# Performance work log

Hardware: AMD Instinct MI355X
Metric: run time of the kernel (lower is better)

The kernel has to match this reference:

```python
import jax, jax.numpy as jnp
import numpy as np

NUM_EXPERTS = 8
TOP_K = 2
HIDDEN = 2048
INTER = 2048
SWIGLU_LIMIT = 7.0
BATCH, SEQ = 4, 2048


def setup_inputs() -> dict:
    key = jax.random.key(0)
    k0, k1, k2, k3, k4 = jax.random.split(key, 5)
    x = jax.random.normal(k0, (BATCH, SEQ, HIDDEN), jnp.float32)
    Wr = jax.random.normal(k1, (HIDDEN, NUM_EXPERTS), jnp.float32) * 0.02
    Wg = jax.random.normal(k2, (NUM_EXPERTS, HIDDEN, INTER), jnp.float32) * 0.02
    Wu = jax.random.normal(k3, (NUM_EXPERTS, HIDDEN, INTER), jnp.float32) * 0.02
    Wd = jax.random.normal(k4, (NUM_EXPERTS, INTER, HIDDEN), jnp.float32) * 0.02
    return {"hidden_states": x, "Wr": Wr, "Wg": Wg, "Wu": Wu, "Wd": Wd}


def reference(hidden_states, Wr, Wg, Wu, Wd):
    # Router: logits [B,S,E], top-k over experts, softmax over the k logits.
    router_logits = jnp.einsum('bsh,he->bse', hidden_states, Wr)
    topk_logits, selected = jax.lax.top_k(router_logits, TOP_K)  # [B,S,K]
    router_probs = jax.nn.softmax(topk_logits, axis=-1)          # [B,S,K]

    # Per-expert masked-dense SwiGLU. Because the Dense layers have no bias,
    # Expert(x * mask) == Expert(x) at selected positions and the combine
    # weight is 0 elsewhere, so running on unmasked x is mathematically
    # identical to the original's masked-input formulation.
    out = jnp.zeros_like(hidden_states)
    for e in range(NUM_EXPERTS):  # fixed structural loop over experts
        w_e = jnp.where(selected == e, router_probs, 0.0).sum(axis=-1, keepdims=True)  # [B,S,1]
        g = jnp.einsum('bsh,hi->bsi', hidden_states, Wg[e])
        g = jnp.clip(jax.nn.silu(g), -SWIGLU_LIMIT, SWIGLU_LIMIT)
        u = jnp.einsum('bsh,hi->bsi', hidden_states, Wu[e])
        h = jnp.einsum('bsi,ih->bsh', g * u, Wd[e])
        out = out + h * w_e
    return out
```

## Files before the change

### kernel.cpp

```cpp
#include <hip/hip_runtime.h>

#define TOKENS 8192
#define HID 2048
#define NEXP 8
#define NT 32
#define MAXTILES 72

typedef float f32x4 __attribute__((ext_vector_type(4)));
typedef short bf16x8 __attribute__((ext_vector_type(8)));

#define WS_XBF     0ULL
#define WS_ACT     33554432ULL
#define WS_WCAT    100663296ULL
#define WS_WDT     234881024ULL
#define WS_ROWTOK  301989888ULL
#define WS_ROWPROB 302055424ULL
#define WS_EIDX    302120960ULL
#define WS_PROBS   302186496ULL
#define WS_META    302252032ULL

__device__ __forceinline__ unsigned short f2bf(float f) {
    union { float f; unsigned int u; } a; a.f = f;
    unsigned int r = a.u + 0x7fffu + ((a.u >> 16) & 1u);
    return (unsigned short)(r >> 16);
}

__device__ __forceinline__ void gload16(void* ldsdst, const void* gsrc) {
    __builtin_amdgcn_global_load_lds(
        (const __attribute__((address_space(1))) void*)gsrc,
        (__attribute__((address_space(3))) void*)ldsdst, 16, 0, 0);
}

#define BAR asm volatile("s_barrier" ::: "memory")
#define VM4 asm volatile("s_waitcnt vmcnt(4)" ::: "memory")
#define VM0 asm volatile("s_waitcnt vmcnt(0)" ::: "memory")

__global__ __launch_bounds__(256) void router_kernel(
    const float* __restrict__ x, const float* __restrict__ Wr,
    unsigned short* __restrict__ xbf, int2* __restrict__ eidx,
    float2* __restrict__ probs, int* __restrict__ meta) {
    __shared__ float wrt[NEXP * HID];
    int tid = threadIdx.x;
    for (int f = tid; f < HID * NEXP; f += 256) {
        int i = f >> 3, e = f & 7;
        wrt[e * HID + i] = Wr[f];
    }
    __syncthreads();
    int w = tid >> 6, l = tid & 63;
    int tok = blockIdx.x * 4 + w;
    const float4* xr = (const float4*)(x + (size_t)tok * HID);
    float acc[NEXP];
#pragma unroll
    for (int e = 0; e < NEXP; ++e) acc[e] = 0.f;
    unsigned long long* xbr = (unsigned long long*)(xbf + (size_t)tok * HID);
#pragma unroll
    for (int it = 0; it < 8; ++it) {
        float4 v = xr[it * 64 + l];
        int k0 = (it * 64 + l) * 4;
#pragma unroll
        for (int e = 0; e < NEXP; ++e) {
            float4 wv = *(const float4*)&wrt[e * HID + k0];
            acc[e] += v.x * wv.x + v.y * wv.y + v.z * wv.z + v.w * wv.w;
        }
        unsigned long long pk = (unsigned long long)f2bf(v.x)
                              | ((unsigned long long)f2bf(v.y) << 16)
                              | ((unsigned long long)f2bf(v.z) << 32)
                              | ((unsigned long long)f2bf(v.w) << 48);
        int qi = ((k0 >> 5) << 3) + (((k0 >> 2) & 3) << 1) + ((k0 >> 4) & 1);
        xbr[qi] = pk;
    }
#pragma unroll
    for (int e = 0; e < NEXP; ++e) {
#pragma unroll
        for (int d = 1; d < 64; d <<= 1) acc[e] += __shfl_xor(acc[e], d, 64);
    }
    if (l == 0) {
        int e0 = 0; float v0 = acc[0];
#pragma unroll
        for (int e = 1; e < NEXP; ++e) if (acc[e] > v0) { v0 = acc[e]; e0 = e; }
        int e1 = -1; float v1 = 0.f;
#pragma unroll
        for (int e = 0; e < NEXP; ++e)
            if (e != e0 && (e1 < 0 || acc[e] > v1)) { v1 = acc[e]; e1 = e; }
        float a = __expf(v1 - v0);
        float inv = 1.f / (1.f + a);
        int2 ei; ei.x = e0; ei.y = e1;
        float2 pp; pp.x = inv; pp.y = a * inv;
        eidx[tok] = ei;
        probs[tok] = pp;
        atomicAdd(&meta[e0], 1);
        atomicAdd(&meta[e1], 1);
    }
}

__global__ __launch_bounds__(256) void convert_kernel(
    const float* __restrict__ Wg, const float* __restrict__ Wu,
    const float* __restrict__ Wd, unsigned short* __restrict__ wcat,
    unsigned short* __restrict__ wdt) {
    int mz = blockIdx.z;
    int mat = mz >> 3, e = mz & 7;
    const float* W = (mat == 0 ? Wg : (mat == 1 ? Wu : Wd)) + (size_t)e * HID * HID;
    int kb = blockIdx.y * 64, nb = blockIdx.x * 64;
    __shared__ unsigned short t[64][68];
    int tid = threadIdx.x;
    int kr = tid >> 4;
    int nc = (tid & 15) * 4;
#pragma unroll
    for (int ki = 0; ki < 4; ++ki) {
        int k = kr + ki * 16;
        float4 v = *(const float4*)&W[(size_t)(kb + k) * HID + nb + nc];
        t[nc + 0][k] = f2bf(v.x);
        t[nc + 1][k] = f2bf(v.y);
        t[nc + 2][k] = f2bf(v.z);
        t[nc + 3][k] = f2bf(v.w);
    }
    __syncthreads();
    int n = tid >> 2;
    int seg = tid & 3;
    int gn = nb + n;
    unsigned short* orow;
    if (mat < 2)
        orow = wcat + ((size_t)e * 4096 + (gn >> 4) * 32 + mat * 16 + (gn & 15)) * HID;
    else
        orow = wdt + ((size_t)e * HID + gn) * HID;
    unsigned long long pk[4];
#pragma unroll
    for (int j = 0; j < 4; ++j) {
        int qi = seg * 4 + j;
        int klocal = ((qi >> 3) << 5) + (((qi >> 1) & 3) << 2) + ((qi & 1) << 4);
        pk[j] = *(const unsigned long long*)&t[n][klocal];
    }
    unsigned long long* dst = (unsigned long long*)&orow[kb + seg * 16];
    dst[0] = pk[0]; dst[1] = pk[1]; dst[2] = pk[2]; dst[3] = pk[3];
}

__global__ void scan_kernel(int* __restrict__ meta) {
    if (threadIdx.x == 0) {
        int s = 0, tiles = 0;
#pragma unroll
        for (int e = 0; e < NEXP; ++e) {
            meta[16 + e] = s;
            int c = meta[e];
            int nt = (c + 255) >> 8;
            for (int i = 0; i < nt && tiles < MAXTILES; ++i)
                meta[32 + tiles++] = (e << 8) | i;
            s += c;
        }
        meta[24] = tiles;
    }
}

__global__ __launch_bounds__(256) void build_kernel(
    const int2* __restrict__ eidx, const float2* __restrict__ probs,
    int* __restrict__ meta, int* __restrict__ row_token, float* __restrict__ row_prob) {
    int t = blockIdx.x * 256 + threadIdx.x;
    if (t >= TOKENS) return;
    int2 e = eidx[t];
    float2 p = probs[t];
    int s0 = meta[16 + e.x] + atomicAdd(&meta[8 + e.x], 1);
    row_token[s0] = t; row_prob[s0] = p.x;
    int s1 = meta[16 + e.y] + atomicAdd(&meta[8 + e.y], 1);
    row_token[s1] = t; row_prob[s1] = p.y;
}

#define STA(dn, kh, tt) { char* _d = lds + (dn)*32768 + (kh)*16384 + tid*16; \
    gload16(_d,        a0 + (tt)*64 + (kh)*32); \
    gload16(_d + 8192, a1 + (tt)*64 + (kh)*32); }
#define STB(dn, kh, tt) { char* _d = lds + (dn)*32768 + 65536 + (kh)*16384 + tid*16; \
    gload16(_d,        b0 + (tt)*64 + (kh)*32); \
    gload16(_d + 8192, b1 + (tt)*64 + (kh)*32); }
#define LDA_TO(dst, d, kh) { const char* _b = lds + (d)*32768 + (kh)*16384 + afo; \
    dst[0] = *(const bf16x8*)(_b);        dst[1] = *(const bf16x8*)(_b + 1024); \
    dst[2] = *(const bf16x8*)(_b + 2048); dst[3] = *(const bf16x8*)(_b + 3072); \
    dst[4] = *(const bf16x8*)(_b + 4096); dst[5] = *(const bf16x8*)(_b + 5120); \
    dst[6] = *(const bf16x8*)(_b + 6144); dst[7] = *(const bf16x8*)(_b + 7168); }
#define LDB(d, kh, nn) (*(const bf16x8*)(lds + (d)*32768 + (kh)*16384 + bfo + (nn)*1024))
#define MM(A, B0, B1, n0, n1) do { \
    __builtin_amdgcn_s_setprio(1); \
    _Pragma("unroll") \
    for (int m = 0; m < 8; ++m) { \
        acc[m][n0] = __builtin_amdgcn_mfma_f32_16x16x32_bf16(A[m], B0, acc[m][n0], 0, 0, 0); \
        acc[m][n1] = __builtin_amdgcn_mfma_f32_16x16x32_bf16(A[m], B1, acc[m][n1], 0, 0, 0); \
    } \
    __builtin_amdgcn_s_setprio(0); \
} while (0)

#define GEMM_MAIN_LOOP \
    f32x4 acc[8][4]; \
    { f32x4 z = {0.f,0.f,0.f,0.f}; \
      _Pragma("unroll") for (int m=0;m<8;++m) \
      _Pragma("unroll") for (int n=0;n<4;++n) acc[m][n]=z; } \
    bf16x8 af[8], af2[8], bq0, bq1, bq2, bq3; \
    STA(0, 0, 0); STB(0, 0, 0); STA(0, 1, 0); STB(0, 1, 0); \
    VM4; BAR; \
    LDA_TO(af, 0, 0); bq0 = LDB(0, 0, 0); bq1 = LDB(0, 0, 1); \
    for (int t = 0; t < NT - 1; ++t) { \
        const int d = t & 1, dn = d ^ 1, tn = t + 1; \
        bq2 = LDB(d, 0, 2); bq3 = LDB(d, 0, 3); \
        STA(dn, 0, tn); \
        MM(af, bq0, bq1, 0, 1); \
        STB(dn, 0, tn); \
        VM4; BAR; \
        LDA_TO(af2, d, 1); bq0 = LDB(d, 1, 0); bq1 = LDB(d, 1, 1); \
        MM(af, bq2, bq3, 2, 3); \
        bq2 = LDB(d, 1, 2); bq3 = LDB(d, 1, 3); \
        STA(dn, 1, tn); \
        MM(af2, bq0, bq1, 0, 1); \
        STB(dn, 1, tn); \
        VM4; BAR; \
        LDA_TO(af, dn, 0); bq0 = LDB(dn, 0, 0); bq1 = LDB(dn, 0, 1); \
        MM(af2, bq2, bq3, 2, 3); \
    } \
    { const int d = (NT - 1) & 1; \
        bq2 = LDB(d, 0, 2); bq3 = LDB(d, 0, 3); \
        MM(af, bq0, bq1, 0, 1); \
        VM0; BAR; \
        LDA_TO(af2, d, 1); bq0 = LDB(d, 1, 0); bq1 = LDB(d, 1, 1); \
        MM(af, bq2, bq3, 2, 3); \
        bq2 = LDB(d, 1, 2); bq3 = LDB(d, 1, 3); \
        MM(af2, bq0, bq1, 0, 1); \
        MM(af2, bq2, bq3, 2, 3); \
    }

__global__ __launch_bounds__(512, 2) void gemm1_kernel(
    const unsigned short* __restrict__ xbf, const unsigned short* __restrict__ wcat,
    const int* __restrict__ row_token, const int* __restrict__ meta,
    unsigned short* __restrict__ act) {
    int id = blockIdx.x;
    int sw = (id & 7) * 144 + (id >> 3);
    int ty = sw % MAXTILES;
    int ct = sw / MAXTILES;
    if (ty >= meta[24]) return;
    int mp = meta[32 + ty];
    int e = mp >> 8, rt = mp & 255;
    int cnt = meta[e];
    int off = meta[16 + e];
    __shared__ __align__(16) char lds[131072];
    int tid = threadIdx.x, w = tid >> 6, l = tid & 63;
    int wr = w >> 2, wc = w & 3;
    int r16 = l & 15, g = l >> 4;

    int srow = tid >> 2;
    int sxu = (tid & 3) ^ ((tid >> 3) & 3);
    int rr0 = rt * 256 + srow;       if (rr0 >= cnt) rr0 = cnt - 1;
    int rr1 = rt * 256 + srow + 128; if (rr1 >= cnt) rr1 = cnt - 1;
    const unsigned short* a0 = xbf + (size_t)row_token[off + rr0] * HID + sxu * 8;
    const unsigned short* a1 = xbf + (size_t)row_token[off + rr1] * HID + sxu * 8;
    const unsigned short* b0 = wcat + ((size_t)(e * 4096 + ct * 256 + srow)) * HID + sxu * 8;
    const unsigned short* b1 = b0 + (size_t)128 * HID;

    int swz = (r16 >> 1) & 3;
    int afo = (wr * 128 + r16) * 64 + (g ^ swz) * 16;
    int bfo = 65536 + (wc * 64 + r16) * 64 + (g ^ swz) * 16;

    GEMM_MAIN_LOOP

    int pb = (ct * 4 + wc) * 32 + (r16 >> 2) * 8 + (r16 & 3);
#pragma unroll
    for (int m = 0; m < 8; ++m) {
        int rbase = wr * 128 + m * 16 + (l >> 4) * 4;
#pragma unroll
        for (int q = 0; q < 4; ++q) {
            int r = rt * 256 + rbase + q;
            if (r < cnt) {
                unsigned short* arow = act + (size_t)(off + r) * HID;
#pragma unroll
                for (int p = 0; p < 2; ++p) {
                    float gg = acc[m][2 * p][q];
                    float uu = acc[m][2 * p + 1][q];
                    float s = gg / (1.f + __expf(-gg));
                    s = fminf(fmaxf(s, -7.f), 7.f);
                    arow[pb + p * 4] = f2bf(s * uu);
                }
            }
        }
    }
}

__global__ __launch_bounds__(512, 2) void gemm2_kernel(
    const unsigned short* __restrict__ act, const unsigned short* __restrict__ wdt,
    const int* __restrict__ row_token, const float* __restrict__ row_prob,
    const int* __restrict__ meta, float* __restrict__ out) {
    int id = blockIdx.x;
    int sw = (id & 7) * 72 + (id >> 3);
    int ty = sw % MAXTILES;
    int ct = sw / MAXTILES;
    if (ty >= meta[24]) return;
    int mp = meta[32 + ty];
    int e = mp >> 8, rt = mp & 255;
    int cnt = meta[e];
    int off = meta[16 + e];
    __shared__ __align__(16) char lds[131072];
    int tid = threadIdx.x, w = tid >> 6, l = tid & 63;
    int wr = w >> 2, wc = w & 3;
    int r16 = l & 15, g = l >> 4;

    int srow = tid >> 2;
    int sxu = (tid & 3) ^ ((tid >> 3) & 3);
    int rr0 = rt * 256 + srow;       if (rr0 >= cnt) rr0 = cnt - 1;
    int rr1 = rt * 256 + srow + 128; if (rr1 >= cnt) rr1 = cnt - 1;
    const unsigned short* a0 = act + (size_t)(off + rr0) * HID + sxu * 8;
    const unsigned short* a1 = act + (size_t)(off + rr1) * HID + sxu * 8;
    const unsigned short* b0 = wdt + ((size_t)(e * HID + ct * 256 + srow)) * HID + sxu * 8;
    const unsigned short* b1 = b0 + (size_t)128 * HID;

    int swz = (r16 >> 1) & 3;
    int afo = (wr * 128 + r16) * 64 + (g ^ swz) * 16;
    int bfo = 65536 + (wc * 64 + r16) * 64 + (g ^ swz) * 16;

    GEMM_MAIN_LOOP

    int colb = ct * 256 + wc * 64;
#pragma unroll
    for (int m = 0; m < 8; ++m) {
        int rbase = wr * 128 + m * 16 + (l >> 4) * 4;
#pragma unroll
        for (int q = 0; q < 4; ++q) {
            int r = rt * 256 + rbase + q;
            if (r < cnt) {
                int slot = off + r;
                int tok = row_token[slot];
                float pr = row_prob[slot];
                float* orow = out + (size_t)tok * HID + colb;
#pragma unroll
                for (int nn = 0; nn < 4; ++nn)
                    unsafeAtomicAdd(&orow[nn * 16 + r16], acc[m][nn][q] * pr);
            }
        }
    }
}

extern "C" void kernel_launch(void* const* d_in, const int* in_sizes, int n_in,
                              void* d_out, int out_size, void* d_ws, size_t ws_size,
                              hipStream_t stream) {
    const float* x  = (const float*)d_in[0];
    const float* Wr = (const float*)d_in[1];
    const float* Wg = (const float*)d_in[2];
    const float* Wu = (const float*)d_in[3];
    const float* Wd = (const float*)d_in[4];
    float* out = (float*)d_out;
    char* ws = (char*)d_ws;

    unsigned short* xbf  = (unsigned short*)(ws + WS_XBF);
    unsigned short* act  = (unsigned short*)(ws + WS_ACT);
    unsigned short* wcat = (unsigned short*)(ws + WS_WCAT);
    unsigned short* wdt  = (unsigned short*)(ws + WS_WDT);
    int* row_token  = (int*)(ws + WS_ROWTOK);
    float* row_prob = (float*)(ws + WS_ROWPROB);
    int2* eidx      = (int2*)(ws + WS_EIDX);
    float2* probs   = (float2*)(ws + WS_PROBS);
    int* meta       = (int*)(ws + WS_META);

    hipMemsetAsync(d_out, 0, (size_t)out_size * sizeof(float), stream);
    hipMemsetAsync(meta, 0, 64, stream);

    hipLaunchKernelGGL(convert_kernel, dim3(32, 32, 24), dim3(256), 0, stream,
                       Wg, Wu, Wd, wcat, wdt);
    hipLaunchKernelGGL(router_kernel, dim3(TOKENS / 4), dim3(256), 0, stream,
                       x, Wr, xbf, eidx, probs, meta);
    hipLaunchKernelGGL(scan_kernel, dim3(1), dim3(64), 0, stream, meta);
    hipLaunchKernelGGL(build_kernel, dim3(TOKENS / 256), dim3(256), 0, stream,
                       eidx, probs, meta, row_token, row_prob);
    hipLaunchKernelGGL(gemm1_kernel, dim3(16 * MAXTILES), dim3(512), 0, stream,
                       xbf, wcat, row_token, meta, act);
    hipLaunchKernelGGL(gemm2_kernel, dim3(8 * MAXTILES), dim3(512), 0, stream,
                       act, wdt, row_token, row_prob, meta, out);
}
```

Measured before the change: 914.5 us.

## Replace gemm2 atomic scatter with bf16 partials and a combine kernel

Measured after the change: 779.2 us. 14.8% less time.

```diff
diff --git a/kernel.cpp b/kernel.cpp
--- a/kernel.cpp
+++ b/kernel.cpp
@@ -18,11 +18,16 @@
 #define WS_EIDX    302120960ULL
 #define WS_PROBS   302186496ULL
 #define WS_META    302252032ULL
+#define WS_SLOT    302253056ULL
 
 __device__ __forceinline__ unsigned short f2bf(float f) {
     union { float f; unsigned int u; } a; a.f = f;
     unsigned int r = a.u + 0x7fffu + ((a.u >> 16) & 1u);
     return (unsigned short)(r >> 16);
+}
+
+__device__ __forceinline__ float bf2f(unsigned int lo16) {
+    union { unsigned int u; float f; } x; x.u = lo16 << 16; return x.f;
 }
 
 __device__ __forceinline__ void gload16(void* ldsdst, const void* gsrc) {
@@ -47,49 +52,52 @@
     }
     __syncthreads();
     int w = tid >> 6, l = tid & 63;
-    int tok = blockIdx.x * 4 + w;
-    const float4* xr = (const float4*)(x + (size_t)tok * HID);
-    float acc[NEXP];
-#pragma unroll
-    for (int e = 0; e < NEXP; ++e) acc[e] = 0.f;
-    unsigned long long* xbr = (unsigned long long*)(xbf + (size_t)tok * HID);
-#pragma unroll
-    for (int it = 0; it < 8; ++it) {
-        float4 v = xr[it * 64 + l];
-        int k0 = (it * 64 + l) * 4;
+#pragma unroll 1
+    for (int ti = 0; ti < 4; ++ti) {
+        int tok = blockIdx.x * 16 + w * 4 + ti;
+        const float4* xr = (const float4*)(x + (size_t)tok * HID);
+        float acc[NEXP];
+#pragma unroll
+        for (int e = 0; e < NEXP; ++e) acc[e] = 0.f;
+        unsigned long long* xbr = (unsigned long long*)(xbf + (size_t)tok * HID);
+#pragma unroll
+        for (int it = 0; it < 8; ++it) {
+            float4 v = xr[it * 64 + l];
+            int k0 = (it * 64 + l) * 4;
+#pragma unroll
+            for (int e = 0; e < NEXP; ++e) {
+                float4 wv = *(const float4*)&wrt[e * HID + k0];
+                acc[e] += v.x * wv.x + v.y * wv.y + v.z * wv.z + v.w * wv.w;
+            }
+            unsigned long long pk = (unsigned long long)f2bf(v.x)
+                                  | ((unsigned long long)f2bf(v.y) << 16)
+                                  | ((unsigned long long)f2bf(v.z) << 32)
+                                  | ((unsigned long long)f2bf(v.w) << 48);
+            int qi = ((k0 >> 5) << 3) + (((k0 >> 2) & 3) << 1) + ((k0 >> 4) & 1);
+            xbr[qi] = pk;
+        }
 #pragma unroll
         for (int e = 0; e < NEXP; ++e) {
-            float4 wv = *(const float4*)&wrt[e * HID + k0];
-            acc[e] += v.x * wv.x + v.y * wv.y + v.z * wv.z + v.w * wv.w;
-        }
-        unsigned long long pk = (unsigned long long)f2bf(v.x)
-                              | ((unsigned long long)f2bf(v.y) << 16)
-                              | ((unsigned long long)f2bf(v.z) << 32)
-                              | ((unsigned long long)f2bf(v.w) << 48);
-        int qi = ((k0 >> 5) << 3) + (((k0 >> 2) & 3) << 1) + ((k0 >> 4) & 1);
-        xbr[qi] = pk;
-    }
-#pragma unroll
-    for (int e = 0; e < NEXP; ++e) {
-#pragma unroll
-        for (int d = 1; d < 64; d <<= 1) acc[e] += __shfl_xor(acc[e], d, 64);
-    }
-    if (l == 0) {
-        int e0 = 0; float v0 = acc[0];
-#pragma unroll
-        for (int e = 1; e < NEXP; ++e) if (acc[e] > v0) { v0 = acc[e]; e0 = e; }
-        int e1 = -1; float v1 = 0.f;
-#pragma unroll
-        for (int e = 0; e < NEXP; ++e)
-            if (e != e0 && (e1 < 0 || acc[e] > v1)) { v1 = acc[e]; e1 = e; }
-        float a = __expf(v1 - v0);
-        float inv = 1.f / (1.f + a);
-        int2 ei; ei.x = e0; ei.y = e1;
-        float2 pp; pp.x = inv; pp.y = a * inv;
-        eidx[tok] = ei;
-        probs[tok] = pp;
-        atomicAdd(&meta[e0], 1);
-        atomicAdd(&meta[e1], 1);
+#pragma unroll
+            for (int d = 1; d < 64; d <<= 1) acc[e] += __shfl_xor(acc[e], d, 64);
+        }
+        if (l == 0) {
+            int e0 = 0; float v0 = acc[0];
+#pragma unroll
+            for (int e = 1; e < NEXP; ++e) if (acc[e] > v0) { v0 = acc[e]; e0 = e; }
+            int e1 = -1; float v1 = 0.f;
+#pragma unroll
+            for (int e = 0; e < NEXP; ++e)
+                if (e != e0 && (e1 < 0 || acc[e] > v1)) { v1 = acc[e]; e1 = e; }
+            float a = __expf(v1 - v0);
+            float inv = 1.f / (1.f + a);
+            int2 ei; ei.x = e0; ei.y = e1;
+            float2 pp; pp.x = inv; pp.y = a * inv;
+            eidx[tok] = ei;
+            probs[tok] = pp;
+            atomicAdd(&meta[e0], 1);
+            atomicAdd(&meta[e1], 1);
+        }
     }
 }
 
@@ -152,15 +160,26 @@
 
 __global__ __launch_bounds__(256) void build_kernel(
     const int2* __restrict__ eidx, const float2* __restrict__ probs,
-    int* __restrict__ meta, int* __restrict__ row_token, float* __restrict__ row_prob) {
-    int t = blockIdx.x * 256 + threadIdx.x;
-    if (t >= TOKENS) return;
+    int* __restrict__ meta, int* __restrict__ row_token, float* __restrict__ row_prob,
+    int2* __restrict__ slots) {
+    __shared__ int lc[NEXP], lbase[NEXP];
+    int tid = threadIdx.x;
+    if (tid < NEXP) lc[tid] = 0;
+    __syncthreads();
+    int t = blockIdx.x * 256 + tid;
     int2 e = eidx[t];
     float2 p = probs[t];
-    int s0 = meta[16 + e.x] + atomicAdd(&meta[8 + e.x], 1);
+    int o0 = atomicAdd(&lc[e.x], 1);
+    int o1 = atomicAdd(&lc[e.y], 1);
+    __syncthreads();
+    if (tid < NEXP) lbase[tid] = atomicAdd(&meta[8 + tid], lc[tid]);
+    __syncthreads();
+    int s0 = meta[16 + e.x] + lbase[e.x] + o0;
+    int s1 = meta[16 + e.y] + lbase[e.y] + o1;
     row_token[s0] = t; row_prob[s0] = p.x;
-    int s1 = meta[16 + e.y] + atomicAdd(&meta[8 + e.y], 1);
     row_token[s1] = t; row_prob[s1] = p.y;
+    int2 sl; sl.x = s0; sl.y = s1;
+    slots[t] = sl;
 }
 
 #define STA(dn, kh, tt) { char* _d = lds + (dn)*32768 + (kh)*16384 + tid*16; \
@@ -279,8 +298,7 @@
 
 __global__ __launch_bounds__(512, 2) void gemm2_kernel(
     const unsigned short* __restrict__ act, const unsigned short* __restrict__ wdt,
-    const int* __restrict__ row_token, const float* __restrict__ row_prob,
-    const int* __restrict__ meta, float* __restrict__ out) {
+    const int* __restrict__ meta, unsigned short* __restrict__ part) {
     int id = blockIdx.x;
     int sw = (id & 7) * 72 + (id >> 3);
     int ty = sw % MAXTILES;
@@ -318,16 +336,37 @@
         for (int q = 0; q < 4; ++q) {
             int r = rt * 256 + rbase + q;
             if (r < cnt) {
-                int slot = off + r;
-                int tok = row_token[slot];
-                float pr = row_prob[slot];
-                float* orow = out + (size_t)tok * HID + colb;
+                unsigned short* prow = part + (size_t)(off + r) * HID + colb;
 #pragma unroll
                 for (int nn = 0; nn < 4; ++nn)
-                    unsafeAtomicAdd(&orow[nn * 16 + r16], acc[m][nn][q] * pr);
+                    prow[nn * 16 + r16] = f2bf(acc[m][nn][q]);
             }
         }
     }
+}
+
+__global__ __launch_bounds__(256) void combine_kernel(
+    const unsigned short* __restrict__ part, const int2* __restrict__ slots,
+    const float2* __restrict__ probs, float* __restrict__ out) {
+    int t = blockIdx.x;
+    int2 s = slots[t];
+    float2 p = probs[t];
+    int c = threadIdx.x * 8;
+    uint4 a = *(const uint4*)(part + (size_t)s.x * HID + c);
+    uint4 b = *(const uint4*)(part + (size_t)s.y * HID + c);
+    unsigned au[4] = {a.x, a.y, a.z, a.w};
+    unsigned bu[4] = {b.x, b.y, b.z, b.w};
+    float res[8];
+#pragma unroll
+    for (int j = 0; j < 4; ++j) {
+        res[2 * j]     = p.x * bf2f(au[j] & 0xffffu) + p.y * bf2f(bu[j] & 0xffffu);
+        res[2 * j + 1] = p.x * bf2f(au[j] >> 16)     + p.y * bf2f(bu[j] >> 16);
+    }
+    float* o = out + (size_t)t * HID + c;
+    float4 o0 = {res[0], res[1], res[2], res[3]};
+    float4 o1 = {res[4], res[5], res[6], res[7]};
+    *(float4*)o = o0;
+    *(float4*)(o + 4) = o1;
 }
 
 extern "C" void kernel_launch(void* const* d_in, const int* in_sizes, int n_in,
@@ -344,25 +383,28 @@
     unsigned short* xbf  = (unsigned short*)(ws + WS_XBF);
     unsigned short* act  = (unsigned short*)(ws + WS_ACT);
     unsigned short* wcat = (unsigned short*)(ws + WS_WCAT);
+    unsigned short* part = (unsigned short*)(ws + WS_WCAT);
     unsigned short* wdt  = (unsigned short*)(ws + WS_WDT);
     int* row_token  = (int*)(ws + WS_ROWTOK);
     float* row_prob = (float*)(ws + WS_ROWPROB);
     int2* eidx      = (int2*)(ws + WS_EIDX);
     float2* probs   = (float2*)(ws + WS_PROBS);
     int* meta       = (int*)(ws + WS_META);
-
-    hipMemsetAsync(d_out, 0, (size_t)out_size * sizeof(float), stream);
+    int2* slots     = (int2*)(ws + WS_SLOT);
+
     hipMemsetAsync(meta, 0, 64, stream);
 
     hipLaunchKernelGGL(convert_kernel, dim3(32, 32, 24), dim3(256), 0, stream,
                        Wg, Wu, Wd, wcat, wdt);
-    hipLaunchKernelGGL(router_kernel, dim3(TOKENS / 4), dim3(256), 0, stream,
+    hipLaunchKernelGGL(router_kernel, dim3(TOKENS / 16), dim3(256), 0, stream,
                        x, Wr, xbf, eidx, probs, meta);
     hipLaunchKernelGGL(scan_kernel, dim3(1), dim3(64), 0, stream, meta);
     hipLaunchKernelGGL(build_kernel, dim3(TOKENS / 256), dim3(256), 0, stream,
-                       eidx, probs, meta, row_token, row_prob);
+                       eidx, probs, meta, row_token, row_prob, slots);
     hipLaunchKernelGGL(gemm1_kernel, dim3(16 * MAXTILES), dim3(512), 0, stream,
                        xbf, wcat, row_token, meta, act);
     hipLaunchKernelGGL(gemm2_kernel, dim3(8 * MAXTILES), dim3(512), 0, stream,
-                       act, wdt, row_token, row_prob, meta, out);
-}
+                       act, wdt, meta, part);
+    hipLaunchKernelGGL(combine_kernel, dim3(TOKENS), dim3(256), 0, stream,
+                       part, slots, probs, out);
+}
```
